# Optimization experiments

Measured on AMD Instinct MI355X. Metric: run time of the kernel, lower is better.

The kernel has to match this reference:

```python
import jax, jax.numpy as jnp
import numpy as np


def setup_inputs() -> dict:
    key = jax.random.key(0)
    k1, k2 = jax.random.split(key)
    f = jax.random.normal(k1, (4, 8192, 3), dtype=jnp.float32)
    f_ = jax.random.normal(k2, (4, 8192, 3), dtype=jnp.float32)
    return {"f": f, "f_": f_}


def _square_distance(src, dst):
    # src: [B,N,3], dst: [B,M,3] -> [B,N,M]
    # ||s-d||^2 = ||s||^2 + ||d||^2 - 2 s.d
    cross = jnp.einsum("bnc,bmc->bnm", src, dst)  # [B,N,M]
    s2 = jnp.sum(src * src, axis=-1)[:, :, None]   # [B,N,1]
    d2 = jnp.sum(dst * dst, axis=-1)[:, None, :]   # [B,1,M]
    return s2 + d2 - 2.0 * cross


def reference(f, f_):
    dis = _square_distance(f, f_)
    dis = jnp.maximum(dis, 0.0)  # dis[dis <= 0] = 0
    f2f_ = jnp.min(dis, axis=2)  # [B,N] nearest in f_ for each point of f
    f_2f = jnp.min(dis, axis=1)  # [B,M] nearest in f for each point of f_
    d = jnp.mean(f2f_, axis=1) + jnp.mean(f_2f, axis=1)  # [B]
    return jnp.mean(d)
```

## Files before the change

kernel.cpp:

```cpp
#include <hip/hip_runtime.h>

#define NPTS  8192
#define BATCH 4

typedef short  bf8    __attribute__((ext_vector_type(8)));
typedef float  f32x16 __attribute__((ext_vector_type(16)));
typedef float  v2f    __attribute__((ext_vector_type(2)));

__device__ inline unsigned short bf16_rne(float x) {
    unsigned u = __float_as_uint(x);
    unsigned r = (u + 0x7FFFu + ((u >> 16) & 1u)) >> 16;
    return (unsigned short)r;
}
__device__ inline float bf16_to_f(unsigned short h) {
    return __uint_as_float(((unsigned)h) << 16);
}
__device__ inline unsigned fenc(float x) {
    unsigned b = __float_as_uint(x);
    return (b & 0x80000000u) ? ~b : (b | 0x80000000u);
}
__device__ inline float fdec(unsigned k) {
    unsigned b = (k & 0x80000000u) ? (k ^ 0x80000000u) : ~k;
    return __uint_as_float(b);
}
template <int CTRL>
__device__ inline float dpp_mov(float x) {
    int i = __float_as_int(x);
    int r = __builtin_amdgcn_update_dpp(i, i, CTRL, 0xF, 0xF, false);
    return __int_as_float(r);
}


__global__ void pack_mfma(const float* __restrict__ f, const float* __restrict__ f_,
                          bf8* __restrict__ fA, bf8* __restrict__ fB,
                          bf8* __restrict__ gA, bf8* __restrict__ gB,
                          unsigned* __restrict__ seg, float* __restrict__ out) {
    int j = blockIdx.x * blockDim.x + threadIdx.x;
    if (j == 0) out[0] = 0.0f;
    seg[j] = 0u;
    int cloud = j >> 15;
    int idx   = j & 32767;
    const float* src = cloud ? f_ : f;
    float x = src[idx * 3 + 0], y = src[idx * 3 + 1], z = src[idx * 3 + 2];
    float w = -0.5f * (x * x + y * y + z * z);
    unsigned short xh = bf16_rne(x), yh = bf16_rne(y), zh = bf16_rne(z);
    unsigned short xl = bf16_rne(x - bf16_to_f(xh));
    unsigned short yl = bf16_rne(y - bf16_to_f(yh));
    unsigned short zl = bf16_rne(z - bf16_to_f(zh));
    unsigned short wh = bf16_rne(w);
    unsigned short wl = bf16_rne(w - bf16_to_f(wh));
    const short ONE = (short)0x3F80;

    bf8 A0, A1, B0, B1;
    A0[0]=(short)xh; A0[1]=(short)yh; A0[2]=(short)zh; A0[3]=(short)xl;
    A0[4]=(short)yl; A0[5]=(short)zl; A0[6]=(short)xh; A0[7]=(short)yh;
    A1[0]=(short)zh; A1[1]=ONE;       A1[2]=ONE;       A1[3]=(short)wh;
    A1[4]=(short)wl; A1[5]=0;         A1[6]=0;         A1[7]=0;
    B0[0]=(short)xh; B0[1]=(short)yh; B0[2]=(short)zh; B0[3]=(short)xh;
    B0[4]=(short)yh; B0[5]=(short)zh; B0[6]=(short)xl; B0[7]=(short)yl;
    B1[0]=(short)zl; B1[1]=(short)wh; B1[2]=(short)wl; B1[3]=ONE;
    B1[4]=ONE;       B1[5]=0;         B1[6]=0;         B1[7]=0;

    int b = idx >> 13, p = idx & 8191;
    int t = p >> 5, li = p & 31;
    size_t base = ((size_t)(b * 256 + t)) * 64;
    bf8* Adst = cloud ? gA : fA;
    bf8* Bdst = cloud ? gB : fB;
    Adst[base + li]      = A0;
    Adst[base + 32 + li] = A1;
    Bdst[base + li]      = B0;
    Bdst[base + 32 + li] = B1;
}

__global__ __launch_bounds__(512, 4) void chamfer_mfma(
        const bf8* __restrict__ fA, const bf8* __restrict__ fB,
        const bf8* __restrict__ gA, const bf8* __restrict__ gB,
        unsigned* __restrict__ seg) {
    __shared__ bf8 lbs[2048];

    int tid  = threadIdx.x;
    int wv   = tid >> 6, lane = tid & 63;
    int bx   = blockIdx.x;
    int mseg = bx & 3;
    int nblk = (bx >> 2) & 15;
    int b    = (bx >> 6) & 3;
    int pass = bx >> 8;

    const bf8* __restrict__ Af = pass ? gA : fA;
    const bf8* __restrict__ Bf = pass ? fB : gB;

    bf8 a[2];
    f32x16 rmax[2];
    int nt_loc = nblk * 16 + wv * 2;
#pragma unroll
    for (int s = 0; s < 2; ++s) {
        a[s] = Af[(size_t)(b * 256 + nt_loc + s) * 64 + lane];
        rmax[s] = (f32x16)(-3.0e38f);
    }

    f32x16 zc = (f32x16)(0.0f);
    for (int c = 0; c < 2; ++c) {
        const bf8* __restrict__ bp =
            Bf + ((size_t)(b * 256 + mseg * 64 + c * 32)) * 64;
        if (c) __syncthreads();
#pragma unroll
        for (int k = 0; k < 4; ++k) lbs[k * 512 + tid] = bp[k * 512 + tid];
        __syncthreads();

        bf8 qa = lbs[lane];
        bf8 qb = lbs[64 + lane];
#pragma unroll 2
        for (int i = 0; i < 16; ++i) {
            int ip = (i + 1) & 15;
            bf8 na = lbs[ip * 128 + lane];
            bf8 nb = lbs[ip * 128 + 64 + lane];
            f32x16 d0 = __builtin_amdgcn_mfma_f32_32x32x16_bf16(a[0], qa, zc, 0, 0, 0);
            f32x16 d1 = __builtin_amdgcn_mfma_f32_32x32x16_bf16(a[0], qb, zc, 0, 0, 0);
            rmax[0] = __builtin_elementwise_max(
                          __builtin_elementwise_max(rmax[0], d0), d1);
            d0 = __builtin_amdgcn_mfma_f32_32x32x16_bf16(a[1], qa, zc, 0, 0, 0);
            d1 = __builtin_amdgcn_mfma_f32_32x32x16_bf16(a[1], qb, zc, 0, 0, 0);
            rmax[1] = __builtin_elementwise_max(
                          __builtin_elementwise_max(rmax[1], d0), d1);
            qa = na; qb = nb;
        }
    }

#pragma unroll
    for (int s = 0; s < 2; ++s) {
#pragma unroll
        for (int r = 0; r < 16; ++r) {
            float x = rmax[s][r];
            x = fmaxf(x, dpp_mov<0xB1>(x));
            x = fmaxf(x, dpp_mov<0x4E>(x));
            x = fmaxf(x, dpp_mov<0x124>(x));
            x = fmaxf(x, dpp_mov<0x128>(x));
            x = fmaxf(x, dpp_mov<0x142>(x));
            rmax[s][r] = x;
        }
    }

    if ((lane & 31) == 16) {
        int rbase = (lane >> 5) * 4;
        unsigned* sg = seg + (size_t)(pass * 4 + b) * NPTS;
#pragma unroll
        for (int s = 0; s < 2; ++s) {
            int n0 = (nt_loc + s) * 32;
#pragma unroll
            for (int r = 0; r < 16; ++r) {
                int row = (r & 3) + 8 * (r >> 2) + rbase;
                atomicMax(&sg[n0 + row], fenc(rmax[s][r]));
            }
        }
    }
}

__global__ __launch_bounds__(1024) void finalize_mfma(
        const unsigned* __restrict__ seg, float* __restrict__ out) {
    __shared__ float partial[16];
    int j = blockIdx.x * 1024 + threadIdx.x;
    float emax = fdec(seg[j]);
    float dist = fmaxf(-2.0f * emax, 0.0f);
    for (int off = 32; off > 0; off >>= 1)
        dist += __shfl_down(dist, off, 64);
    int lane = threadIdx.x & 63, wv = threadIdx.x >> 6;
    if (lane == 0) partial[wv] = dist;
    __syncthreads();
    if (threadIdx.x < 16) {
        float s = partial[threadIdx.x];
        for (int off = 8; off > 0; off >>= 1)
            s += __shfl_down(s, off, 64);
        if (threadIdx.x == 0) atomicAdd(out, s * (1.0f / 32768.0f));
    }
}


__global__ void pack_pk(const float* __restrict__ f, const float* __restrict__ f_,
                        float4* __restrict__ pk, float* __restrict__ prf,
                        float* __restrict__ out) {
    int j = blockIdx.x * blockDim.x + threadIdx.x;
    if (j == 0) out[0] = 0.0f;
    const float* src = (j >= 32768) ? f_ : f;
    int idx = j & 32767;
    float x = src[idx * 3 + 0], y = src[idx * 3 + 1], z = src[idx * 3 + 2];
    float w = -0.5f * (x * x + y * y + z * z);
    pk[j] = make_float4(x, y, z, w);
    int  slot = j & 1;
    long base = (long)(j >> 1) * 8;
    prf[base + 0 + slot] = x;
    prf[base + 2 + slot] = y;
    prf[base + 4 + slot] = z;
    prf[base + 6 + slot] = w;
}

__global__ __launch_bounds__(512, 8) void chamfer_pk(
        const float4* __restrict__ pk, const float4* __restrict__ pr,
        float* __restrict__ seg) {
    __shared__ float red[8][256];
    int tid  = threadIdx.x;
    int wv   = __builtin_amdgcn_readfirstlane(tid >> 6);
    int lane = tid & 63;
    int bx   = blockIdx.x;
    int tile = bx & 31;
    int b    = (bx >> 5) & 3;
    int dir  = (bx >> 7) & 1;
    int mq   = bx >> 8;

    const float4* __restrict__ A = pk + ((size_t)dir * BATCH + b) * NPTS;
    int n_base = tile * 256;
    v2f px[4], py[4], pz[4], e2[4];
#pragma unroll
    for (int r = 0; r < 4; ++r) {
        float4 p = A[n_base + lane + 64 * r];
        px[r] = (v2f){p.x, p.x};
        py[r] = (v2f){p.y, p.y};
        pz[r] = (v2f){p.z, p.z};
        e2[r] = (v2f){-1e30f, -1e30f};
    }
    int sb_m = (1 - dir) * BATCH + b;
    const float4* __restrict__ mp =
        pr + ((size_t)sb_m * 4096 + mq * 1024 + wv * 128) * 2;

    for (int i = 0; i < 128; i += 4) {
#pragma unroll
        for (int u = 0; u < 4; ++u) {
            float4 qa = mp[(i + u) * 2 + 0];
            float4 qb = mp[(i + u) * 2 + 1];
            v2f qx = (v2f){qa.x, qa.y};
            v2f qy = (v2f){qa.z, qa.w};
            v2f qz = (v2f){qb.x, qb.y};
            v2f qw = (v2f){qb.z, qb.w};
#pragma unroll
            for (int r = 0; r < 4; ++r) {
                v2f c = __builtin_elementwise_fma(px[r], qx, qw);
                c = __builtin_elementwise_fma(py[r], qy, c);
                c = __builtin_elementwise_fma(pz[r], qz, c);
                e2[r] = __builtin_elementwise_max(e2[r], c);
            }
        }
    }
#pragma unroll
    for (int r = 0; r < 4; ++r)
        red[wv][lane + 64 * r] = fmaxf(e2[r].x, e2[r].y);
    __syncthreads();
    if (tid < 256) {
        float emax = red[0][tid];
#pragma unroll
        for (int ww = 1; ww < 8; ++ww) emax = fmaxf(emax, red[ww][tid]);
        seg[mq * (2 * BATCH * NPTS) + dir * (BATCH * NPTS) + b * NPTS
            + n_base + tid] = emax;
    }
}

__global__ __launch_bounds__(1024) void finalize_pk(
        const float4* __restrict__ pk, const float* __restrict__ seg,
        float* __restrict__ out) {
    __shared__ float partial[16];
    int j = blockIdx.x * 1024 + threadIdx.x;
    float emax = seg[j];
#pragma unroll
    for (int q = 1; q < 4; ++q) emax = fmaxf(emax, seg[q * 65536 + j]);
    float dist = fmaxf(-2.0f * (emax + pk[j].w), 0.0f);
    for (int off = 32; off > 0; off >>= 1)
        dist += __shfl_down(dist, off, 64);
    int lane = threadIdx.x & 63, wv = threadIdx.x >> 6;
    if (lane == 0) partial[wv] = dist;
    __syncthreads();
    if (threadIdx.x < 16) {
        float s = partial[threadIdx.x];
        for (int off = 8; off > 0; off >>= 1)
            s += __shfl_down(s, off, 64);
        if (threadIdx.x == 0) atomicAdd(out, s * (1.0f / 32768.0f));
    }
}


__global__ void zero_out_kernel(float* __restrict__ out) { out[0] = 0.0f; }

__global__ __launch_bounds__(1024) void chamfer_fallback(
        const float* __restrict__ f, const float* __restrict__ f_,
        float* __restrict__ out) {
    __shared__ float wlds[NPTS];
    __shared__ float red[16][256];
    __shared__ float partial[4];
    int tid  = threadIdx.x;
    int wv   = __builtin_amdgcn_readfirstlane(tid >> 6);
    int lane = tid & 63;
    int bx   = blockIdx.x;
    int dir  = bx >> 7;
    int b    = (bx >> 5) & 3;
    int tile = bx & 31;
    int n_base = tile * 256;
    const float* __restrict__ A  = dir ? f_ : f;
    const float* __restrict__ Bm = dir ? f  : f_;
    const float* an = A  + (size_t)b * NPTS * 3;
    const float* bm = Bm + (size_t)b * NPTS * 3;
    for (int i = tid; i < NPTS; i += 1024) {
        float x = bm[i * 3 + 0], y = bm[i * 3 + 1], z = bm[i * 3 + 2];
        wlds[i] = -0.5f * (x * x + y * y + z * z);
    }
    float xn[4], yn[4], zn[4];
#pragma unroll
    for (int r = 0; r < 4; ++r) {
        int n = n_base + lane + 64 * r;
        xn[r] = an[n * 3 + 0]; yn[r] = an[n * 3 + 1]; zn[r] = an[n * 3 + 2];
    }
    __syncthreads();
    float e[4];
#pragma unroll
    for (int r = 0; r < 4; ++r) e[r] = -1e30f;
    int m0 = wv * (NPTS / 16);
#pragma unroll 4
    for (int i = 0; i < NPTS / 16; ++i) {
        int m = m0 + i;
        float qx = bm[m * 3 + 0], qy = bm[m * 3 + 1], qz = bm[m * 3 + 2];
        float qw = wlds[m];
#pragma unroll
        for (int r = 0; r < 4; ++r) {
            float c = fmaf(zn[r], qz, fmaf(yn[r], qy, fmaf(xn[r], qx, qw)));
            e[r] = fmaxf(e[r], c);
        }
    }
#pragma unroll
    for (int r = 0; r < 4; ++r) red[wv][lane + 64 * r] = e[r];
    __syncthreads();
    if (tid < 256) {
        float emax = red[0][tid];
#pragma unroll
        for (int ww = 1; ww < 16; ++ww) emax = fmaxf(emax, red[ww][tid]);
        int n = n_base + tid;
        float x = an[n * 3 + 0], y = an[n * 3 + 1], z = an[n * 3 + 2];
        float dist = fmaxf(x * x + y * y + z * z - 2.0f * emax, 0.0f);
        for (int off = 32; off > 0; off >>= 1)
            dist += __shfl_down(dist, off, 64);
        if ((tid & 63) == 0) partial[tid >> 6] = dist;
    }
    __syncthreads();
    if (tid == 0) {
        float s = partial[0] + partial[1] + partial[2] + partial[3];
        atomicAdd(out, s * (1.0f / 32768.0f));
    }
}

extern "C" void kernel_launch(void* const* d_in, const int* in_sizes, int n_in,
                              void* d_out, int out_size, void* d_ws, size_t ws_size,
                              hipStream_t stream) {
    const float* f  = (const float*)d_in[0];
    const float* f_ = (const float*)d_in[1];
    float* out = (float*)d_out;

    const size_t MB = 1048576;
    if (ws_size >= 5 * MB) {
        bf8*      fA  = (bf8*)d_ws;
        bf8*      fB  = (bf8*)((char*)d_ws + 1 * MB);
        bf8*      gA  = (bf8*)((char*)d_ws + 2 * MB);
        bf8*      gB  = (bf8*)((char*)d_ws + 3 * MB);
        unsigned* seg = (unsigned*)((char*)d_ws + 4 * MB);
        pack_mfma<<<256, 256, 0, stream>>>(f, f_, fA, fB, gA, gB, seg, out);
        chamfer_mfma<<<512, 512, 0, stream>>>(fA, fB, gA, gB, seg);
        finalize_mfma<<<64, 1024, 0, stream>>>(seg, out);
    } else if (ws_size >= 3 * MB) {
        float4* pk = (float4*)d_ws;
        float4* pr = (float4*)((char*)d_ws + 1 * MB);
        float*  sg = (float*)((char*)d_ws + 2 * MB);
        pack_pk<<<256, 256, 0, stream>>>(f, f_, pk, (float*)pr, out);
        chamfer_pk<<<1024, 512, 0, stream>>>(pk, pr, sg);
        finalize_pk<<<64, 1024, 0, stream>>>(pk, sg, out);
    } else {
        zero_out_kernel<<<1, 1, 0, stream>>>(out);
        chamfer_fallback<<<256, 1024, 0, stream>>>(f, f_, out);
    }
}
```

Before: 84.91 us.

## Compute both chamfer directions from one MFMA distance pass with column-max LDS accumulation

The kernel previously ran two passes (f→f_ and f_→f), each computing the full distance matrix with MFMA. Now a single pass computes each tile once. It keeps the existing row-max reduction and adds per-tile column maxima, which are reduced in registers and accumulated via LDS atomicMax, then flushed to global with atomics. This halves the MFMA work and the packed data, at the cost of extra VALU reductions, LDS atomics inside the inner loop, and sched_barriers that may limit overlap.

```diff
diff --git a/kernel.cpp b/kernel.cpp
--- a/kernel.cpp
+++ b/kernel.cpp
@@ -29,11 +29,19 @@
     int r = __builtin_amdgcn_update_dpp(i, i, CTRL, 0xF, 0xF, false);
     return __int_as_float(r);
 }
+__device__ inline float redmax16(f32x16 v) {
+    float a = fmaxf(v[0], v[1]),  b = fmaxf(v[2], v[3]);
+    float c = fmaxf(v[4], v[5]),  d = fmaxf(v[6], v[7]);
+    float e = fmaxf(v[8], v[9]),  f = fmaxf(v[10], v[11]);
+    float g = fmaxf(v[12], v[13]), h = fmaxf(v[14], v[15]);
+    float ab = fmaxf(a, b), cd = fmaxf(c, d);
+    float ef = fmaxf(e, f), gh = fmaxf(g, h);
+    return fmaxf(fmaxf(ab, cd), fmaxf(ef, gh));
+}
 
 
 __global__ void pack_mfma(const float* __restrict__ f, const float* __restrict__ f_,
-                          bf8* __restrict__ fA, bf8* __restrict__ fB,
-                          bf8* __restrict__ gA, bf8* __restrict__ gB,
+                          bf8* __restrict__ fA, bf8* __restrict__ gB,
                           unsigned* __restrict__ seg, float* __restrict__ out) {
     int j = blockIdx.x * blockDim.x + threadIdx.x;
     if (j == 0) out[0] = 0.0f;
@@ -51,79 +59,81 @@
     unsigned short wl = bf16_rne(w - bf16_to_f(wh));
     const short ONE = (short)0x3F80;
 
-    bf8 A0, A1, B0, B1;
-    A0[0]=(short)xh; A0[1]=(short)yh; A0[2]=(short)zh; A0[3]=(short)xl;
-    A0[4]=(short)yl; A0[5]=(short)zl; A0[6]=(short)xh; A0[7]=(short)yh;
-    A1[0]=(short)zh; A1[1]=ONE;       A1[2]=ONE;       A1[3]=(short)wh;
-    A1[4]=(short)wl; A1[5]=0;         A1[6]=0;         A1[7]=0;
-    B0[0]=(short)xh; B0[1]=(short)yh; B0[2]=(short)zh; B0[3]=(short)xh;
-    B0[4]=(short)yh; B0[5]=(short)zh; B0[6]=(short)xl; B0[7]=(short)yl;
-    B1[0]=(short)zl; B1[1]=(short)wh; B1[2]=(short)wl; B1[3]=ONE;
-    B1[4]=ONE;       B1[5]=0;         B1[6]=0;         B1[7]=0;
-
     int b = idx >> 13, p = idx & 8191;
     int t = p >> 5, li = p & 31;
     size_t base = ((size_t)(b * 256 + t)) * 64;
-    bf8* Adst = cloud ? gA : fA;
-    bf8* Bdst = cloud ? gB : fB;
-    Adst[base + li]      = A0;
-    Adst[base + 32 + li] = A1;
-    Bdst[base + li]      = B0;
-    Bdst[base + 32 + li] = B1;
+    if (cloud == 0) {
+        bf8 A0, A1;
+        A0[0]=(short)xh; A0[1]=(short)yh; A0[2]=(short)zh; A0[3]=(short)xl;
+        A0[4]=(short)yl; A0[5]=(short)zl; A0[6]=(short)xh; A0[7]=(short)yh;
+        A1[0]=(short)zh; A1[1]=ONE;       A1[2]=ONE;       A1[3]=(short)wh;
+        A1[4]=(short)wl; A1[5]=0;         A1[6]=0;         A1[7]=0;
+        fA[base + li]      = A0;
+        fA[base + 32 + li] = A1;
+    } else {
+        bf8 B0, B1;
+        B0[0]=(short)xh; B0[1]=(short)yh; B0[2]=(short)zh; B0[3]=(short)xh;
+        B0[4]=(short)yh; B0[5]=(short)zh; B0[6]=(short)xl; B0[7]=(short)yl;
+        B1[0]=(short)zl; B1[1]=(short)wh; B1[2]=(short)wl; B1[3]=ONE;
+        B1[4]=ONE;       B1[5]=0;         B1[6]=0;         B1[7]=0;
+        gB[base + li]      = B0;
+        gB[base + 32 + li] = B1;
+    }
 }
 
 __global__ __launch_bounds__(512, 4) void chamfer_mfma(
-        const bf8* __restrict__ fA, const bf8* __restrict__ fB,
-        const bf8* __restrict__ gA, const bf8* __restrict__ gB,
+        const bf8* __restrict__ fA, const bf8* __restrict__ gB,
         unsigned* __restrict__ seg) {
     __shared__ bf8 lbs[2048];
+    __shared__ unsigned colacc[1024];
 
     int tid  = threadIdx.x;
     int wv   = tid >> 6, lane = tid & 63;
     int bx   = blockIdx.x;
-    int mseg = bx & 3;
-    int nblk = (bx >> 2) & 15;
-    int b    = (bx >> 6) & 3;
-    int pass = bx >> 8;
-
-    const bf8* __restrict__ Af = pass ? gA : fA;
-    const bf8* __restrict__ Bf = pass ? fB : gB;
+    int mseg = bx & 7;
+    int nblk = (bx >> 3) & 15;
+    int b    = bx >> 7;
 
     bf8 a[2];
     f32x16 rmax[2];
     int nt_loc = nblk * 16 + wv * 2;
 #pragma unroll
     for (int s = 0; s < 2; ++s) {
-        a[s] = Af[(size_t)(b * 256 + nt_loc + s) * 64 + lane];
+        a[s] = fA[(size_t)(b * 256 + nt_loc + s) * 64 + lane];
         rmax[s] = (f32x16)(-3.0e38f);
     }
 
+    const bf8* __restrict__ bp = gB + ((size_t)(b * 256 + mseg * 32)) * 64;
+#pragma unroll
+    for (int k = 0; k < 4; ++k) lbs[k * 512 + tid] = bp[k * 512 + tid];
+    colacc[tid]       = 0u;
+    colacc[tid + 512] = 0u;
+    __syncthreads();
+
     f32x16 zc = (f32x16)(0.0f);
-    for (int c = 0; c < 2; ++c) {
-        const bf8* __restrict__ bp =
-            Bf + ((size_t)(b * 256 + mseg * 64 + c * 32)) * 64;
-        if (c) __syncthreads();
-#pragma unroll
-        for (int k = 0; k < 4; ++k) lbs[k * 512 + tid] = bp[k * 512 + tid];
-        __syncthreads();
-
-        bf8 qa = lbs[lane];
-        bf8 qb = lbs[64 + lane];
+    unsigned* cp = &colacc[lane & 31];
+    bf8 qa = lbs[lane];
+    bf8 qb = lbs[64 + lane];
 #pragma unroll 2
-        for (int i = 0; i < 16; ++i) {
-            int ip = (i + 1) & 15;
-            bf8 na = lbs[ip * 128 + lane];
-            bf8 nb = lbs[ip * 128 + 64 + lane];
-            f32x16 d0 = __builtin_amdgcn_mfma_f32_32x32x16_bf16(a[0], qa, zc, 0, 0, 0);
-            f32x16 d1 = __builtin_amdgcn_mfma_f32_32x32x16_bf16(a[0], qb, zc, 0, 0, 0);
-            rmax[0] = __builtin_elementwise_max(
-                          __builtin_elementwise_max(rmax[0], d0), d1);
-            d0 = __builtin_amdgcn_mfma_f32_32x32x16_bf16(a[1], qa, zc, 0, 0, 0);
-            d1 = __builtin_amdgcn_mfma_f32_32x32x16_bf16(a[1], qb, zc, 0, 0, 0);
-            rmax[1] = __builtin_elementwise_max(
-                          __builtin_elementwise_max(rmax[1], d0), d1);
-            qa = na; qb = nb;
-        }
+    for (int i = 0; i < 16; ++i) {
+        int ip = (i + 1) & 15;
+        bf8 na = lbs[ip * 128 + lane];
+        bf8 nb = lbs[ip * 128 + 64 + lane];
+        f32x16 d00 = __builtin_amdgcn_mfma_f32_32x32x16_bf16(a[0], qa, zc, 0, 0, 0);
+        f32x16 d01 = __builtin_amdgcn_mfma_f32_32x32x16_bf16(a[0], qb, zc, 0, 0, 0);
+        rmax[0] = __builtin_elementwise_max(
+                      __builtin_elementwise_max(rmax[0], d00), d01);
+        float t00 = redmax16(d00);
+        float t01 = redmax16(d01);
+        __builtin_amdgcn_sched_barrier(0);
+        f32x16 d10 = __builtin_amdgcn_mfma_f32_32x32x16_bf16(a[1], qa, zc, 0, 0, 0);
+        f32x16 d11 = __builtin_amdgcn_mfma_f32_32x32x16_bf16(a[1], qb, zc, 0, 0, 0);
+        rmax[1] = __builtin_elementwise_max(
+                      __builtin_elementwise_max(rmax[1], d10), d11);
+        atomicMax(cp + i * 64,      fenc(fmaxf(t00, redmax16(d10))));
+        atomicMax(cp + i * 64 + 32, fenc(fmaxf(t01, redmax16(d11))));
+        __builtin_amdgcn_sched_barrier(0);
+        qa = na; qb = nb;
     }
 
 #pragma unroll
@@ -142,7 +152,7 @@
 
     if ((lane & 31) == 16) {
         int rbase = (lane >> 5) * 4;
-        unsigned* sg = seg + (size_t)(pass * 4 + b) * NPTS;
+        unsigned* sg = seg + (size_t)b * NPTS;
 #pragma unroll
         for (int s = 0; s < 2; ++s) {
             int n0 = (nt_loc + s) * 32;
@@ -152,6 +162,13 @@
                 atomicMax(&sg[n0 + row], fenc(rmax[s][r]));
             }
         }
+    }
+
+    __syncthreads();
+    {
+        unsigned* sg = seg + (size_t)(4 + b) * NPTS + mseg * 1024;
+        atomicMax(&sg[tid],       colacc[tid]);
+        atomicMax(&sg[tid + 512], colacc[tid + 512]);
     }
 }
 
@@ -352,12 +369,10 @@
     const size_t MB = 1048576;
     if (ws_size >= 5 * MB) {
         bf8*      fA  = (bf8*)d_ws;
-        bf8*      fB  = (bf8*)((char*)d_ws + 1 * MB);
-        bf8*      gA  = (bf8*)((char*)d_ws + 2 * MB);
-        bf8*      gB  = (bf8*)((char*)d_ws + 3 * MB);
-        unsigned* seg = (unsigned*)((char*)d_ws + 4 * MB);
-        pack_mfma<<<256, 256, 0, stream>>>(f, f_, fA, fB, gA, gB, seg, out);
-        chamfer_mfma<<<512, 512, 0, stream>>>(fA, fB, gA, gB, seg);
+        bf8*      gB  = (bf8*)((char*)d_ws + 1 * MB);
+        unsigned* seg = (unsigned*)((char*)d_ws + 2 * MB);
+        pack_mfma<<<256, 256, 0, stream>>>(f, f_, fA, gB, seg, out);
+        chamfer_mfma<<<512, 512, 0, stream>>>(fA, gB, seg);
         finalize_mfma<<<64, 1024, 0, stream>>>(seg, out);
     } else if (ws_size >= 3 * MB) {
         float4* pk = (float4*)d_ws;
```

Measured after the change: 84.15 us. Within noise of the previous version (-0.9%).
